# Kernel tuning notes

Hardware: AMD Instinct MI355X
Metric: run time of the kernel (lower is better)

The kernel has to match this reference:

```python
import jax, jax.numpy as jnp
import numpy as np

N_P, N_G, E, E_LBL = 100000, 40000, 1600000, 500000
D, F_GO, L = 64, 1000, 3

def setup_inputs() -> dict:
    key = jax.random.key(0)
    ks = jax.random.split(key, 16)
    s = 0.05
    return {
        'go_x': jax.random.normal(ks[0], (N_G, F_GO), jnp.float32),
        'protein_emb': jax.random.normal(ks[1], (N_P, D), jnp.float32) * s,
        'go_emb': jax.random.normal(ks[2], (N_G, D), jnp.float32) * s,
        'lin_W': jax.random.normal(ks[3], (F_GO, D), jnp.float32) * s,
        'lin_b': jnp.zeros((D,), jnp.float32),
        'Wl': jax.random.normal(ks[4], (L, 2, D, D), jnp.float32) * s,
        'bl': jnp.zeros((L, 2, D), jnp.float32),
        'Wr': jax.random.normal(ks[5], (L, 2, D, D), jnp.float32) * s,
        'protein_nid': jnp.arange(N_P, dtype=jnp.int32),
        'go_nid': jnp.arange(N_G, dtype=jnp.int32),
        'src_pg': jax.random.randint(ks[6], (E,), 0, N_P, jnp.int32),
        'dst_pg': jax.random.randint(ks[7], (E,), 0, N_G, jnp.int32),
        'src_gp': jax.random.randint(ks[8], (E,), 0, N_G, jnp.int32),
        'dst_gp': jax.random.randint(ks[9], (E,), 0, N_P, jnp.int32),
        'label_src': jax.random.randint(ks[10], (E_LBL,), 0, N_P, jnp.int32),
        'label_dst': jax.random.randint(ks[11], (E_LBL,), 0, N_G, jnp.int32),
    }

def _mean_aggr(x_src, src, dst, n_dst):
    # gather source features per edge, scatter-mean to destination nodes
    msg = jax.ops.segment_sum(x_src[src], dst, num_segments=n_dst)
    cnt = jax.ops.segment_sum(jnp.ones_like(dst, dtype=x_src.dtype), dst, num_segments=n_dst)
    return msg / jnp.maximum(cnt, 1.0)[:, None]

def reference(go_x, protein_emb, go_emb, lin_W, lin_b, Wl, bl, Wr,
              protein_nid, go_nid, src_pg, dst_pg, src_gp, dst_gp,
              label_src, label_dst):
    # input embeddings
    xp = protein_emb[protein_nid]                      # [N_P, D]
    xg = go_x @ lin_W + lin_b + go_emb[go_nid]         # [N_G, D]
    np_, ng_ = xp.shape[0], xg.shape[0]
    for l in range(L):
        # edge type 0: protein -> go_term; edge type 1: go_term -> protein
        agg_g = _mean_aggr(xp, src_pg, dst_pg, ng_)
        agg_p = _mean_aggr(xg, src_gp, dst_gp, np_)
        new_g = agg_g @ Wl[l, 0] + bl[l, 0] + xg @ Wr[l, 0]
        new_p = agg_p @ Wl[l, 1] + bl[l, 1] + xp @ Wr[l, 1]
        if l < L - 1:  # ReLU after conv1/conv2 only (dropout = identity at eval)
            new_g = jax.nn.relu(new_g)
            new_p = jax.nn.relu(new_p)
        xp, xg = new_p, new_g
    # Classifier: per-label-edge dot product
    return (xp[label_src] * xg[label_dst]).sum(axis=-1)  # [E_LBL]
```

## Files before the change

### kernel.cpp

```cpp
#include <hip/hip_runtime.h>

#define DD 64
constexpr int N_P   = 100000;
constexpr int N_G   = 40000;
constexpr int NE    = 1600000;
constexpr int E_LBL = 500000;
constexpr int F_GO  = 1000;
constexpr int KSTEPS = 32;

constexpr int SHIFT_G = 8;
constexpr int NB_G    = (N_G + 255) >> 8;
constexpr int SHIFT_P = 9;
constexpr int NB_P    = (N_P + 511) >> 9;
constexpr int NB_MAX  = 256;
constexpr int W_MAX   = 512;
constexpr int CHUNK   = 8192;

typedef __attribute__((ext_vector_type(8))) short bf16x8;
typedef __attribute__((ext_vector_type(4))) float f32x4;
typedef __attribute__((ext_vector_type(4))) short s16x4;

__device__ __forceinline__ unsigned short f2bf_rne(float x) {
    unsigned u = __float_as_uint(x);
    u += 0x7fff + ((u >> 16) & 1);
    return (unsigned short)(u >> 16);
}
__device__ __forceinline__ float bf2f(unsigned short h) {
    return __uint_as_float((unsigned)h << 16);
}
struct BfPair { short h; short l; };
__device__ __forceinline__ BfPair split_bf(float x) {
    BfPair p;
    unsigned short hh = f2bf_rne(x);
    unsigned short ll = f2bf_rne(x - bf2f(hh));
    p.h = (short)hh; p.l = (short)ll;
    return p;
}

__global__ void gather_rows(const float* __restrict__ emb, const int* __restrict__ nid,
                            float* __restrict__ out, int n) {
    int t = blockIdx.x * blockDim.x + threadIdx.x;
    int total = n * (DD / 4);
    if (t >= total) return;
    int row = t / (DD / 4);
    int c4  = t % (DD / 4);
    int srow = nid[row];
    reinterpret_cast<float4*>(out)[(size_t)row * (DD / 4) + c4] =
        reinterpret_cast<const float4*>(emb)[(size_t)srow * (DD / 4) + c4];
}

__global__ void pack_B(const float* __restrict__ lin_W,
                       short* __restrict__ BH, short* __restrict__ BL) {
    int t = blockIdx.x * blockDim.x + threadIdx.x;
    if (t >= KSTEPS * 64 * 4) return;
    int s = t >> 8, n = (t >> 2) & 63, q = t & 3;
    int base = t * 8;
#pragma unroll
    for (int j = 0; j < 8; ++j) {
        int k = s * 32 + q * 8 + j;
        float v = (k < F_GO) ? lin_W[(size_t)k * 64 + n] : 0.f;
        BfPair p = split_bf(v);
        BH[base + j] = p.h;
        BL[base + j] = p.l;
    }
}

__global__ __launch_bounds__(256) void lin_go_part(const float* __restrict__ go_x,
        const short* __restrict__ BH, const short* __restrict__ BL,
        float* __restrict__ part0, float* __restrict__ part1) {
    int tid = threadIdx.x;
    int wave = tid >> 6, lane = tid & 63;
    int ml = lane & 15, q = lane >> 4;
    int half = blockIdx.x & 1;
    int row0 = (blockIdx.x >> 1) * 64 + wave * 16;
    float* outp = half ? part1 : part0;
    const float* arow = go_x + (size_t)(row0 + ml) * F_GO;
    f32x4 acc[4] = {};
    int s0 = half * 16;
    for (int s = s0; s < s0 + 16; ++s) {
        int kb = s * 32 + q * 8;
        int kc = kb > 992 ? 992 : kb;
        float4 va = *reinterpret_cast<const float4*>(arow + kc);
        float4 vb = *reinterpret_cast<const float4*>(arow + kc + 4);
        bf16x8 ah, al;
        {
            BfPair p0 = split_bf(va.x), p1 = split_bf(va.y),
                   p2 = split_bf(va.z), p3 = split_bf(va.w);
            BfPair p4 = split_bf(vb.x), p5 = split_bf(vb.y),
                   p6 = split_bf(vb.z), p7 = split_bf(vb.w);
            ah[0]=p0.h; ah[1]=p1.h; ah[2]=p2.h; ah[3]=p3.h;
            ah[4]=p4.h; ah[5]=p5.h; ah[6]=p6.h; ah[7]=p7.h;
            al[0]=p0.l; al[1]=p1.l; al[2]=p2.l; al[3]=p3.l;
            al[4]=p4.l; al[5]=p5.l; al[6]=p6.l; al[7]=p7.l;
        }
#pragma unroll
        for (int nt = 0; nt < 4; ++nt) {
            int off = ((s * 64 + nt * 16 + ml) * 4 + q) * 8;
            bf16x8 bh = *reinterpret_cast<const bf16x8*>(BH + off);
            bf16x8 bl = *reinterpret_cast<const bf16x8*>(BL + off);
            acc[nt] = __builtin_amdgcn_mfma_f32_16x16x32_bf16(ah, bh, acc[nt], 0, 0, 0);
            acc[nt] = __builtin_amdgcn_mfma_f32_16x16x32_bf16(al, bh, acc[nt], 0, 0, 0);
            acc[nt] = __builtin_amdgcn_mfma_f32_16x16x32_bf16(ah, bl, acc[nt], 0, 0, 0);
        }
    }
#pragma unroll
    for (int reg = 0; reg < 4; ++reg) {
        int row = row0 + q * 4 + reg;
#pragma unroll
        for (int nt = 0; nt < 4; ++nt) {
            int col = nt * 16 + ml;
            outp[(size_t)row * 64 + col] = acc[nt][reg];
        }
    }
}

__global__ void lin_go_reduce(float* __restrict__ g0, const float* __restrict__ g1,
        const float* __restrict__ lin_b, const float* __restrict__ go_emb,
        const int* __restrict__ go_nid) {
    int t = blockIdx.x * blockDim.x + threadIdx.x;
    if (t >= N_G * 16) return;
    int row = t >> 4;
    int c4  = (t & 15) * 4;
    int nid = go_nid[row];
    float4 a  = *reinterpret_cast<const float4*>(g0 + (size_t)row * 64 + c4);
    float4 b  = *reinterpret_cast<const float4*>(g1 + (size_t)row * 64 + c4);
    float4 bb = *reinterpret_cast<const float4*>(lin_b + c4);
    float4 ee = *reinterpret_cast<const float4*>(go_emb + (size_t)nid * 64 + c4);
    float4 r;
    r.x = a.x + b.x + bb.x + ee.x;
    r.y = a.y + b.y + bb.y + ee.y;
    r.z = a.z + b.z + bb.z + ee.z;
    r.w = a.w + b.w + bb.w + ee.w;
    *reinterpret_cast<float4*>(g0 + (size_t)row * 64 + c4) = r;
}

__global__ __launch_bounds__(256) void bin_count(const int* __restrict__ dst,
        int* __restrict__ cnt, int nE, int shift, int nb) {
    __shared__ int h[NB_MAX];
    for (int i = threadIdx.x; i < nb; i += 256) h[i] = 0;
    __syncthreads();
    for (int e = blockIdx.x * blockDim.x + threadIdx.x; e < nE; e += gridDim.x * blockDim.x)
        atomicAdd(&h[dst[e] >> shift], 1);
    __syncthreads();
    for (int i = threadIdx.x; i < nb; i += 256)
        if (h[i]) atomicAdd(&cnt[i], h[i]);
}

__global__ __launch_bounds__(256) void scan_buckets(const int* __restrict__ cnt,
        int* __restrict__ base, int* __restrict__ cursor, int nb, int total) {
    __shared__ int sh[NB_MAX];
    int v = (threadIdx.x < nb) ? cnt[threadIdx.x] : 0;
    sh[threadIdx.x] = v;
    __syncthreads();
    for (int off = 1; off < NB_MAX; off <<= 1) {
        int t = (threadIdx.x >= off) ? sh[threadIdx.x - off] : 0;
        __syncthreads();
        sh[threadIdx.x] += t;
        __syncthreads();
    }
    if (threadIdx.x < nb) {
        int ex = sh[threadIdx.x] - v;
        base[threadIdx.x] = ex;
        cursor[threadIdx.x] = ex;
    }
    if (threadIdx.x == 0) base[nb] = total;
}

__global__ __launch_bounds__(256) void bin_fill(const int* __restrict__ src,
        const int* __restrict__ dst, int* __restrict__ cursor,
        int2* __restrict__ binned, int nE, int shift, int nb) {
    __shared__ int hist[NB_MAX];
    __shared__ int base[NB_MAX];
    int e0 = blockIdx.x * CHUNK;
    int e1 = e0 + CHUNK; if (e1 > nE) e1 = nE;
    for (int i = threadIdx.x; i < nb; i += 256) hist[i] = 0;
    __syncthreads();
    for (int e = e0 + threadIdx.x; e < e1; e += 256)
        atomicAdd(&hist[dst[e] >> shift], 1);
    __syncthreads();
    for (int i = threadIdx.x; i < nb; i += 256) {
        int c = hist[i];
        base[i] = c ? atomicAdd(&cursor[i], c) : 0;
        hist[i] = 0;
    }
    __syncthreads();
    for (int e = e0 + threadIdx.x; e < e1; e += 256) {
        int d = dst[e];
        int b = d >> shift;
        int slot = base[b] + atomicAdd(&hist[b], 1);
        binned[slot] = make_int2(src[e], d);
    }
}

__global__ __launch_bounds__(256) void bucket_to_csr(const int2* __restrict__ binned,
        const int* __restrict__ bbase, int* __restrict__ rowptr, int* __restrict__ csr_src,
        int n, int shift, int nE) {
    int b = blockIdx.x;
    int W = 1 << shift;
    int mask = W - 1;
    __shared__ int hist[W_MAX];
    __shared__ int curs[W_MAX];
    int s = bbase[b], e = bbase[b + 1];
    for (int i = threadIdx.x; i < W; i += 256) hist[i] = 0;
    __syncthreads();
    for (int i = s + threadIdx.x; i < e; i += 256)
        atomicAdd(&hist[binned[i].y & mask], 1);
    __syncthreads();
    for (int i = threadIdx.x; i < W; i += 256) curs[i] = hist[i];
    __syncthreads();
    for (int off = 1; off < W; off <<= 1) {
        int i0 = threadIdx.x, i1 = threadIdx.x + 256;
        int t0 = (i0 >= off && i0 < W) ? curs[i0 - off] : 0;
        int t1 = (i1 >= off && i1 < W) ? curs[i1 - off] : 0;
        __syncthreads();
        if (i0 < W) curs[i0] += t0;
        if (i1 < W) curs[i1] += t1;
        __syncthreads();
    }
    int row0 = b << shift;
    for (int j = threadIdx.x; j < W; j += 256) {
        int start = s + curs[j] - hist[j];
        hist[j] = start;
        int r = row0 + j;
        if (r < n) rowptr[r] = start;
    }
    if (b == 0 && threadIdx.x == 0) rowptr[n] = nE;
    __syncthreads();
    for (int i = s + threadIdx.x; i < e; i += 256) {
        int2 ed = binned[i];
        int slot = atomicAdd(&hist[ed.y & mask], 1);
        csr_src[slot] = ed.x;
    }
}

__global__ void aggregate_csr(const float* __restrict__ x, const int* __restrict__ rowptr,
                              const int* __restrict__ csr_src, float* __restrict__ out, int n) {
    int row = blockIdx.x * 4 + (threadIdx.x >> 6);
    if (row >= n) return;
    int lane = threadIdx.x & 63;
    int qg   = lane >> 4;
    int l16  = lane & 15;
    int s = rowptr[row], e = rowptr[row + 1];
    const float4* x4 = reinterpret_cast<const float4*>(x);
    float4 a0 = make_float4(0.f, 0.f, 0.f, 0.f);
    float4 a1 = make_float4(0.f, 0.f, 0.f, 0.f);
    int i = s + qg;
    for (; i + 4 < e; i += 8) {
        int s0 = csr_src[i];
        int s1 = csr_src[i + 4];
        float4 v0 = x4[(size_t)s0 * 16 + l16];
        float4 v1 = x4[(size_t)s1 * 16 + l16];
        a0.x += v0.x; a0.y += v0.y; a0.z += v0.z; a0.w += v0.w;
        a1.x += v1.x; a1.y += v1.y; a1.z += v1.z; a1.w += v1.w;
    }
    if (i < e) {
        int s0 = csr_src[i];
        float4 v0 = x4[(size_t)s0 * 16 + l16];
        a0.x += v0.x; a0.y += v0.y; a0.z += v0.z; a0.w += v0.w;
    }
    a0.x += a1.x; a0.y += a1.y; a0.z += a1.z; a0.w += a1.w;
    a0.x += __shfl_xor(a0.x, 16); a0.y += __shfl_xor(a0.y, 16);
    a0.z += __shfl_xor(a0.z, 16); a0.w += __shfl_xor(a0.w, 16);
    a0.x += __shfl_xor(a0.x, 32); a0.y += __shfl_xor(a0.y, 32);
    a0.z += __shfl_xor(a0.z, 32); a0.w += __shfl_xor(a0.w, 32);
    if (qg == 0) {
        float inv = (e > s) ? 1.0f / (float)(e - s) : 0.0f;
        float4 r = make_float4(a0.x * inv, a0.y * inv, a0.z * inv, a0.w * inv);
        reinterpret_cast<float4*>(out)[(size_t)row * 16 + l16] = r;
    }
}

constexpr int LDA_UN = 72;
__global__ __launch_bounds__(256) void update_nodes_mfma(
        const float* agg, const float* __restrict__ x,
        const float* __restrict__ Wl, const float* __restrict__ bias,
        const float* __restrict__ Wr, float* out, int n, int relu) {
    __shared__ short Ah[64][LDA_UN], Al[64][LDA_UN];
    __shared__ short Bh[64][LDA_UN], Bl[64][LDA_UN];
    int tid = threadIdx.x;
    int wave = tid >> 6, lane = tid & 63;
    int ml = lane & 15, q = lane >> 4;
    int row0 = blockIdx.x * 64;
    f32x4 acc[4] = {};
    for (int half = 0; half < 2; ++half) {
        const float* Xsrc = half ? x : agg;
        const float* Wsrc = half ? Wr : Wl;
        {
            int k4 = tid & 15;
            for (int r = tid >> 4; r < 64; r += 16) {
                int grow = row0 + r; if (grow >= n) grow = n - 1;
                float4 v = *reinterpret_cast<const float4*>(&Xsrc[(size_t)grow * 64 + k4 * 4]);
                s16x4 h, l;
                BfPair p0 = split_bf(v.x), p1 = split_bf(v.y),
                       p2 = split_bf(v.z), p3 = split_bf(v.w);
                h[0] = p0.h; h[1] = p1.h; h[2] = p2.h; h[3] = p3.h;
                l[0] = p0.l; l[1] = p1.l; l[2] = p2.l; l[3] = p3.l;
                *reinterpret_cast<s16x4*>(&Ah[r][k4 * 4]) = h;
                *reinterpret_cast<s16x4*>(&Al[r][k4 * 4]) = l;
            }
        }
        {
            int nn = tid & 63;
            for (int kr = tid >> 6; kr < 64; kr += 4) {
                float v = Wsrc[(size_t)kr * 64 + nn];
                BfPair p = split_bf(v);
                Bh[nn][kr] = p.h; Bl[nn][kr] = p.l;
            }
        }
        __syncthreads();
#pragma unroll
        for (int kc = 0; kc < 64; kc += 32) {
            int kb = kc + q * 8;
            int m = wave * 16 + ml;
            bf16x8 ah = *reinterpret_cast<const bf16x8*>(&Ah[m][kb]);
            bf16x8 al = *reinterpret_cast<const bf16x8*>(&Al[m][kb]);
#pragma unroll
            for (int nt = 0; nt < 4; ++nt) {
                int nn = nt * 16 + ml;
                bf16x8 bh = *reinterpret_cast<const bf16x8*>(&Bh[nn][kb]);
                bf16x8 bl = *reinterpret_cast<const bf16x8*>(&Bl[nn][kb]);
                acc[nt] = __builtin_amdgcn_mfma_f32_16x16x32_bf16(ah, bh, acc[nt], 0, 0, 0);
                acc[nt] = __builtin_amdgcn_mfma_f32_16x16x32_bf16(al, bh, acc[nt], 0, 0, 0);
                acc[nt] = __builtin_amdgcn_mfma_f32_16x16x32_bf16(ah, bl, acc[nt], 0, 0, 0);
            }
        }
        __syncthreads();
    }
#pragma unroll
    for (int reg = 0; reg < 4; ++reg) {
        int row = row0 + wave * 16 + q * 4 + reg;
        if (row >= n) continue;
#pragma unroll
        for (int nt = 0; nt < 4; ++nt) {
            int col = nt * 16 + ml;
            float v = acc[nt][reg] + bias[col];
            if (relu) v = fmaxf(v, 0.0f);
            out[(size_t)row * 64 + col] = v;
        }
    }
}

__global__ void classify(const float* __restrict__ xp, const float* __restrict__ xg,
                         const int* __restrict__ ls, const int* __restrict__ ld,
                         float* __restrict__ out, int nE) {
    int t = blockIdx.x * blockDim.x + threadIdx.x;
    int e = t >> 4;
    int l16 = t & 15;
    if (e >= nE) return;
    int s = ls[e], d = ld[e];
    float4 a = reinterpret_cast<const float4*>(xp)[(size_t)s * 16 + l16];
    float4 b = reinterpret_cast<const float4*>(xg)[(size_t)d * 16 + l16];
    float v = a.x * b.x + a.y * b.y + a.z * b.z + a.w * b.w;
    v += __shfl_xor(v, 8);
    v += __shfl_xor(v, 4);
    v += __shfl_xor(v, 2);
    v += __shfl_xor(v, 1);
    if (l16 == 0) out[e] = v;
}

extern "C" void kernel_launch(void* const* d_in, const int* in_sizes, int n_in,
                              void* d_out, int out_size, void* d_ws, size_t ws_size,
                              hipStream_t stream) {
    const float* go_x        = (const float*)d_in[0];
    const float* protein_emb = (const float*)d_in[1];
    const float* go_emb      = (const float*)d_in[2];
    const float* lin_W       = (const float*)d_in[3];
    const float* lin_b       = (const float*)d_in[4];
    const float* Wl          = (const float*)d_in[5];
    const float* bl          = (const float*)d_in[6];
    const float* Wr          = (const float*)d_in[7];
    const int* protein_nid   = (const int*)d_in[8];
    const int* go_nid        = (const int*)d_in[9];
    const int* src_pg        = (const int*)d_in[10];
    const int* dst_pg        = (const int*)d_in[11];
    const int* src_gp        = (const int*)d_in[12];
    const int* dst_gp        = (const int*)d_in[13];
    const int* label_src     = (const int*)d_in[14];
    const int* label_dst     = (const int*)d_in[15];
    float* out = (float*)d_out;

    float* ws = (float*)d_ws;
    float* p0 = ws;
    float* p1 = p0 + (size_t)N_P * 64;
    float* g0 = p1 + (size_t)N_P * 64;
    float* g1 = g0 + (size_t)N_G * 64;
    int* ib = (int*)(g1 + (size_t)N_G * 64);
    int* rowptr_g  = ib;  ib += N_G + 1;
    int* rowptr_p  = ib;  ib += N_P + 1;
    int* bucket_cnt    = ib;  ib += NB_MAX;
    int* bucket_base   = ib;  ib += NB_MAX + 1;
    int* bucket_cursor = ib;  ib += NB_MAX;
    int* csr_g = ib;  ib += NE;
    int* csr_p = ib;  ib += NE;
    short* BfragH = (short*)ib;
    short* BfragL = BfragH + KSTEPS * 64 * 4 * 8;
    int2* binned = (int2*)p1;

    gather_rows<<<(N_P * (DD / 4) + 255) / 256, 256, 0, stream>>>(protein_emb, protein_nid, p0, N_P);
    pack_B<<<(KSTEPS * 64 * 4 + 255) / 256, 256, 0, stream>>>(lin_W, BfragH, BfragL);
    lin_go_part<<<2 * (N_G / 64), 256, 0, stream>>>(go_x, BfragH, BfragL, g0, g1);
    lin_go_reduce<<<(N_G * 16 + 255) / 256, 256, 0, stream>>>(g0, g1, lin_b, go_emb, go_nid);

    int nblk_fill = (NE + CHUNK - 1) / CHUNK;

    hipMemsetAsync(bucket_cnt, 0, NB_MAX * sizeof(int), stream);
    bin_count<<<256, 256, 0, stream>>>(dst_pg, bucket_cnt, NE, SHIFT_G, NB_G);
    scan_buckets<<<1, 256, 0, stream>>>(bucket_cnt, bucket_base, bucket_cursor, NB_G, NE);
    bin_fill<<<nblk_fill, 256, 0, stream>>>(src_pg, dst_pg, bucket_cursor, binned, NE, SHIFT_G, NB_G);
    bucket_to_csr<<<NB_G, 256, 0, stream>>>(binned, bucket_base, rowptr_g, csr_g, N_G, SHIFT_G, NE);

    hipMemsetAsync(bucket_cnt, 0, NB_MAX * sizeof(int), stream);
    bin_count<<<256, 256, 0, stream>>>(dst_gp, bucket_cnt, NE, SHIFT_P, NB_P);
    scan_buckets<<<1, 256, 0, stream>>>(bucket_cnt, bucket_base, bucket_cursor, NB_P, NE);
    bin_fill<<<nblk_fill, 256, 0, stream>>>(src_gp, dst_gp, bucket_cursor, binned, NE, SHIFT_P, NB_P);
    bucket_to_csr<<<NB_P, 256, 0, stream>>>(binned, bucket_base, rowptr_p, csr_p, N_P, SHIFT_P, NE);

    float* xp = p0; float* xg = g0; float* sp = p1; float* sg = g1;
    for (int l = 0; l < 3; ++l) {
        aggregate_csr<<<(N_G + 3) / 4, 256, 0, stream>>>(xp, rowptr_g, csr_g, sg, N_G);
        aggregate_csr<<<(N_P + 3) / 4, 256, 0, stream>>>(xg, rowptr_p, csr_p, sp, N_P);
        int relu = (l < 2) ? 1 : 0;
        const float* wl0 = Wl + (size_t)(l * 2 + 0) * 4096;
        const float* wl1 = Wl + (size_t)(l * 2 + 1) * 4096;
        const float* wr0 = Wr + (size_t)(l * 2 + 0) * 4096;
        const float* wr1 = Wr + (size_t)(l * 2 + 1) * 4096;
        const float* b0  = bl + (size_t)(l * 2 + 0) * 64;
        const float* b1  = bl + (size_t)(l * 2 + 1) * 64;
        update_nodes_mfma<<<(N_G + 63) / 64, 256, 0, stream>>>(sg, xg, wl0, b0, wr0, sg, N_G, relu);
        update_nodes_mfma<<<(N_P + 63) / 64, 256, 0, stream>>>(sp, xp, wl1, b1, wr1, sp, N_P, relu);
        float* t;
        t = xp; xp = sp; sp = t;
        t = xg; xg = sg; sg = t;
    }
    classify<<<(E_LBL * 16 + 255) / 256, 256, 0, stream>>>(xp, xg, label_src, label_dst, out, E_LBL);
}
```

Baseline: 946.1 us.

## Merge both aggregations into one launch with one 16-lane group per row

The two per-edge-type CSR mean aggregations are combined into a single kernel launch that covers go rows followed by protein rows. Each destination row is now handled by a 16-thread group that walks all of its edges serially, with an 8-way unrolled gather across four accumulators, instead of a 64-lane wave that split edges four ways and reduced with shuffles. This removes one launch and the cross-lane reduction, and raises rows per block to improve memory-level parallelism. The trade-off is a longer serial chain per row and possible load imbalance from rows with higher degree. The grid size relies on N_G+N_P being divisible by 16.

Result: no change. 939.1 us (-0.7%).

```diff
diff --git a/kernel.cpp b/kernel.cpp
--- a/kernel.cpp
+++ b/kernel.cpp
@@ -233,41 +233,58 @@
     }
 }
 
-__global__ void aggregate_csr(const float* __restrict__ x, const int* __restrict__ rowptr,
-                              const int* __restrict__ csr_src, float* __restrict__ out, int n) {
-    int row = blockIdx.x * 4 + (threadIdx.x >> 6);
-    if (row >= n) return;
-    int lane = threadIdx.x & 63;
-    int qg   = lane >> 4;
-    int l16  = lane & 15;
-    int s = rowptr[row], e = rowptr[row + 1];
-    const float4* x4 = reinterpret_cast<const float4*>(x);
+__global__ __launch_bounds__(256) void aggregate_both(
+        const float* __restrict__ xp, const float* __restrict__ xg,
+        const int* __restrict__ rowptr_g, const int* __restrict__ csr_g,
+        const int* __restrict__ rowptr_p, const int* __restrict__ csr_p,
+        float* __restrict__ sg, float* __restrict__ sp) {
+    int grp = (blockIdx.x << 4) + (threadIdx.x >> 4);
+    int l16 = threadIdx.x & 15;
+    const float4* x4; const int* rp; const int* cs; float* o; int row;
+    if (grp < N_G) {
+        x4 = reinterpret_cast<const float4*>(xp);
+        rp = rowptr_g; cs = csr_g; o = sg; row = grp;
+    } else {
+        x4 = reinterpret_cast<const float4*>(xg);
+        rp = rowptr_p; cs = csr_p; o = sp; row = grp - N_G;
+    }
+    int s = rp[row], e = rp[row + 1];
     float4 a0 = make_float4(0.f, 0.f, 0.f, 0.f);
     float4 a1 = make_float4(0.f, 0.f, 0.f, 0.f);
-    int i = s + qg;
-    for (; i + 4 < e; i += 8) {
-        int s0 = csr_src[i];
-        int s1 = csr_src[i + 4];
+    float4 a2 = make_float4(0.f, 0.f, 0.f, 0.f);
+    float4 a3 = make_float4(0.f, 0.f, 0.f, 0.f);
+    int i = s;
+    for (; i + 8 <= e; i += 8) {
+        int s0 = cs[i],     s1 = cs[i + 1], s2 = cs[i + 2], s3 = cs[i + 3];
+        int s4 = cs[i + 4], s5 = cs[i + 5], s6 = cs[i + 6], s7 = cs[i + 7];
         float4 v0 = x4[(size_t)s0 * 16 + l16];
         float4 v1 = x4[(size_t)s1 * 16 + l16];
+        float4 v2 = x4[(size_t)s2 * 16 + l16];
+        float4 v3 = x4[(size_t)s3 * 16 + l16];
+        float4 v4 = x4[(size_t)s4 * 16 + l16];
+        float4 v5 = x4[(size_t)s5 * 16 + l16];
+        float4 v6 = x4[(size_t)s6 * 16 + l16];
+        float4 v7 = x4[(size_t)s7 * 16 + l16];
         a0.x += v0.x; a0.y += v0.y; a0.z += v0.z; a0.w += v0.w;
         a1.x += v1.x; a1.y += v1.y; a1.z += v1.z; a1.w += v1.w;
-    }
-    if (i < e) {
-        int s0 = csr_src[i];
+        a2.x += v2.x; a2.y += v2.y; a2.z += v2.z; a2.w += v2.w;
+        a3.x += v3.x; a3.y += v3.y; a3.z += v3.z; a3.w += v3.w;
+        a0.x += v4.x; a0.y += v4.y; a0.z += v4.z; a0.w += v4.w;
+        a1.x += v5.x; a1.y += v5.y; a1.z += v5.z; a1.w += v5.w;
+        a2.x += v6.x; a2.y += v6.y; a2.z += v6.z; a2.w += v6.w;
+        a3.x += v7.x; a3.y += v7.y; a3.z += v7.z; a3.w += v7.w;
+    }
+    for (; i < e; ++i) {
+        int s0 = cs[i];
         float4 v0 = x4[(size_t)s0 * 16 + l16];
         a0.x += v0.x; a0.y += v0.y; a0.z += v0.z; a0.w += v0.w;
     }
     a0.x += a1.x; a0.y += a1.y; a0.z += a1.z; a0.w += a1.w;
-    a0.x += __shfl_xor(a0.x, 16); a0.y += __shfl_xor(a0.y, 16);
-    a0.z += __shfl_xor(a0.z, 16); a0.w += __shfl_xor(a0.w, 16);
-    a0.x += __shfl_xor(a0.x, 32); a0.y += __shfl_xor(a0.y, 32);
-    a0.z += __shfl_xor(a0.z, 32); a0.w += __shfl_xor(a0.w, 32);
-    if (qg == 0) {
-        float inv = (e > s) ? 1.0f / (float)(e - s) : 0.0f;
-        float4 r = make_float4(a0.x * inv, a0.y * inv, a0.z * inv, a0.w * inv);
-        reinterpret_cast<float4*>(out)[(size_t)row * 16 + l16] = r;
-    }
+    a2.x += a3.x; a2.y += a3.y; a2.z += a3.z; a2.w += a3.w;
+    a0.x += a2.x; a0.y += a2.y; a0.z += a2.z; a0.w += a2.w;
+    float inv = (e > s) ? 1.0f / (float)(e - s) : 0.0f;
+    float4 r = make_float4(a0.x * inv, a0.y * inv, a0.z * inv, a0.w * inv);
+    reinterpret_cast<float4*>(o)[(size_t)row * 16 + l16] = r;
 }
 
 constexpr int LDA_UN = 72;
@@ -417,8 +434,8 @@
 
     float* xp = p0; float* xg = g0; float* sp = p1; float* sg = g1;
     for (int l = 0; l < 3; ++l) {
-        aggregate_csr<<<(N_G + 3) / 4, 256, 0, stream>>>(xp, rowptr_g, csr_g, sg, N_G);
-        aggregate_csr<<<(N_P + 3) / 4, 256, 0, stream>>>(xg, rowptr_p, csr_p, sp, N_P);
+        aggregate_both<<<(N_G + N_P) / 16, 256, 0, stream>>>(
+            xp, xg, rowptr_g, csr_g, rowptr_p, csr_p, sg, sp);
         int relu = (l < 2) ? 1 : 0;
         const float* wl0 = Wl + (size_t)(l * 2 + 0) * 4096;
         const float* wl1 = Wl + (size_t)(l * 2 + 1) * 4096;
```
